# Kernel tuning notes

Measured on AMD Instinct MI355X. Metric: run time of the kernel, lower is better.

The kernel has to match this reference:

```python
import jax, jax.numpy as jnp
import numpy as np
from jax import lax

C = 768
CA = C // 4  # adapter_channels = 192
L = 197      # 1 CLS + 14*14 patches
T_FRAMES = 16
B = 16
N = B * T_FRAMES


def quick_gelu(x):
    return x * jax.nn.sigmoid(1.702 * x)


def setup_inputs() -> dict:
    key = jax.random.key(0)
    ks = jax.random.split(key, 16)
    s = 0.02
    return {
        "x": jax.random.normal(ks[0], (L, N, C), dtype=jnp.float32),
        "T": T_FRAMES,
        # main path (fc1 -> depthwise conv1d over T -> fc2)
        "fc1_w": jax.random.normal(ks[1], (C, CA), jnp.float32) * s,
        "fc1_b": jnp.zeros((CA,), jnp.float32),
        "conv_w": jax.random.normal(ks[2], (CA, 1, 3), jnp.float32) * s,  # (O, I/g, K)
        "conv_b": jnp.zeros((CA,), jnp.float32),
        "fc2_w": jax.random.normal(ks[3], (CA, C), jnp.float32) * s,
        "fc2_b": jnp.zeros((C,), jnp.float32),
        # offset adapter (fc1 -> depthwise conv3d (1,3,3) -> fc2)
        "off_fc1_w": jax.random.normal(ks[4], (C, CA), jnp.float32) * s,
        "off_fc1_b": jnp.zeros((CA,), jnp.float32),
        "off_conv_w": jax.random.normal(ks[5], (CA, 1, 1, 3, 3), jnp.float32) * s,  # (O, I/g, D, H, W)
        "off_conv_b": jnp.zeros((CA,), jnp.float32),
        "off_fc2_w": jax.random.normal(ks[6], (CA, C), jnp.float32) * s,
        "off_fc2_b": jnp.zeros((C,), jnp.float32),
        # mlp branch (c_in -> QuickGELU -> c_out)
        "mlp_in_w": jax.random.normal(ks[7], (C, CA), jnp.float32) * s,
        "mlp_in_b": jnp.zeros((CA,), jnp.float32),
        "mlp_out_w": jax.random.normal(ks[8], (CA, C), jnp.float32) * s,
        "mlp_out_b": jnp.zeros((C,), jnp.float32),
    }


def _offset_adapter(x, T, fc1_w, fc1_b, conv_w, conv_b, fc2_w, fc2_b):
    Lx, Nx, Cx = x.shape
    Bx = Nx // T
    HW = Lx - 1
    H = int(round(HW ** 0.5))
    Ca = fc1_w.shape[1]
    xp = jnp.transpose(x, (1, 0, 2))            # (N, L, C)
    xs = xp[:, 1:, :].reshape(Bx, T, HW, Cx)    # (B, T, HW, C)
    # former frame: index [0, 0, 1, ..., T-2]
    x_former = jnp.concatenate([xs[:, :1], xs[:, :-1]], axis=1)
    off = xs - x_former
    off = off @ fc1_w + fc1_b                   # (B, T, HW, Ca)
    off = off.reshape(Bx, T, H, H, Ca).transpose(0, 4, 1, 2, 3)  # (B, Ca, T, H, W)
    off = lax.conv_general_dilated(
        off, conv_w, window_strides=(1, 1, 1),
        padding=[(0, 0), (1, 1), (1, 1)],
        dimension_numbers=("NCDHW", "OIDHW", "NCDHW"),
        feature_group_count=Ca,
    ) + conv_b[None, :, None, None, None]
    off = off.transpose(0, 2, 3, 4, 1).reshape(Nx, HW, Ca)
    off = off @ fc2_w + fc2_b                   # (N, L-1, C)
    return jnp.transpose(off, (1, 0, 2))        # (L-1, N, C)


def reference(x, T, fc1_w, fc1_b, conv_w, conv_b, fc2_w, fc2_b,
              off_fc1_w, off_fc1_b, off_conv_w, off_conv_b, off_fc2_w, off_fc2_b,
              mlp_in_w, mlp_in_b, mlp_out_w, mlp_out_b):
    Lx, Nx, Cx = x.shape
    Bx = Nx // T
    Ca = fc1_w.shape[1]

    offset = _offset_adapter(x, T, off_fc1_w, off_fc1_b, off_conv_w, off_conv_b,
                             off_fc2_w, off_fc2_b)  # (L-1, N, C)

    # mlp identity branch
    x_id = quick_gelu(x @ mlp_in_w + mlp_in_b) @ mlp_out_w + mlp_out_b  # (L, N, C)

    # main branch: fc1 -> depthwise conv1d along T -> fc2
    h = x @ fc1_w + fc1_b                                   # (L, N, Ca)
    h = jnp.transpose(h, (1, 0, 2)).reshape(Bx, T, Lx, Ca)  # (B, T, L, Ca)
    h = h.transpose(0, 2, 3, 1).reshape(Bx * Lx, Ca, T)     # (B*L, Ca, T)
    h = lax.conv_general_dilated(
        h, conv_w, window_strides=(1,), padding=[(1, 1)],
        dimension_numbers=("NCH", "OIH", "NCH"),
        feature_group_count=Ca,
    ) + conv_b[None, :, None]
    h = h.transpose(0, 2, 1).reshape(Bx, Lx, T, Ca)
    h = h.transpose(0, 2, 1, 3).reshape(Nx, Lx, Ca)
    h = jnp.transpose(h, (1, 0, 2))                         # (L, N, Ca)
    h = h @ fc2_w + fc2_b                                   # (L, N, C)

    x_id = x_id.at[1:].add(offset)
    return h + x_id
```

## Files before the change

### kernel.cpp

```cpp
#include <hip/hip_runtime.h>

#define L_DIM 197
#define N_DIM 256
#define C_DIM 768
#define CA_DIM 192
#define M_DIM (L_DIM * N_DIM)

typedef short s16x8 __attribute__((ext_vector_type(8)));
typedef float f32x4 __attribute__((ext_vector_type(4)));

__device__ __forceinline__ unsigned short f2bf(float f) {
  unsigned x = __builtin_bit_cast(unsigned, f);
  x = (x + 0x7fffu + ((x >> 16) & 1u)) >> 16;
  return (unsigned short)x;
}
__device__ __forceinline__ float bflo(unsigned u) { return __builtin_bit_cast(float, u << 16); }
__device__ __forceinline__ float bfhi(unsigned u) { return __builtin_bit_cast(float, u & 0xffff0000u); }

__device__ __forceinline__ void unp8(uint4 v, float* f) {
  f[0] = bflo(v.x); f[1] = bfhi(v.x); f[2] = bflo(v.y); f[3] = bfhi(v.y);
  f[4] = bflo(v.z); f[5] = bfhi(v.z); f[6] = bflo(v.w); f[7] = bfhi(v.w);
}

__device__ __forceinline__ void mfma16(f32x4& acc, s16x8 a, s16x8 b) {
  asm("v_mfma_f32_16x16x32_bf16 %0, %1, %2, %0" : "+v"(acc) : "v"(a), "v"(b));
}

typedef const void __attribute__((address_space(1)))* gp_t;
typedef void __attribute__((address_space(3)))* lp_t;
__device__ __forceinline__ void gl16(const void* g, void* l) {
  __builtin_amdgcn_global_load_lds((gp_t)g, (lp_t)l, 16, 0, 0);
}

__device__ __forceinline__ int swz(int pid, int nwg) {
  const int q = nwg >> 3, r = nwg & 7, x = pid & 7, s = pid >> 3;
  return (x < r ? x * (q + 1) : r * (q + 1) + (x - r) * q) + s;
}

__global__ __launch_bounds__(256) void prep_k(
    const float* __restrict__ fc1_w, const float* __restrict__ mlp_in_w,
    const float* __restrict__ off_fc1_w, const float* __restrict__ fc2_w,
    const float* __restrict__ mlp_out_w, const float* __restrict__ off_fc2_w,
    unsigned short* __restrict__ wa, unsigned short* __restrict__ wc) {
  __shared__ float t[32][33];
  const int b = blockIdx.x;
  const int job = b / 144, tt = b - job * 144;
  const float* in = job == 0 ? fc1_w : job == 1 ? mlp_in_w : job == 2 ? off_fc1_w
                  : job == 3 ? fc2_w : job == 4 ? mlp_out_w : off_fc2_w;
  const int Cc = job < 3 ? 192 : 768;
  const int tc = Cc >> 5;
  const int tr0 = (tt / tc) << 5, tc0 = (tt - (tt / tc) * tc) << 5;
  const int lr = threadIdx.x >> 5, lc = threadIdx.x & 31;
#pragma unroll
  for (int p = 0; p < 4; p++)
    t[p * 8 + lr][lc] = in[(tr0 + p * 8 + lr) * Cc + tc0 + lc];
  __syncthreads();
#pragma unroll
  for (int p = 0; p < 4; p++) {
    const int orow = tc0 + p * 8 + lr;
    const int ocol = tr0 + lc;
    const unsigned short v = f2bf(t[lc][p * 8 + lr]);
    if (job < 3) wa[(job * 192 + orow) * 768 + ocol] = v;
    else         wc[orow * 576 + (job - 3) * 192 + ocol] = v;
  }
}

__global__ __launch_bounds__(256, 1) void gemm_a_k(
    const float* __restrict__ x, const unsigned short* __restrict__ wa,
    const float* __restrict__ fc1_b, const float* __restrict__ mlp_in_b,
    unsigned short* __restrict__ h1, unsigned short* __restrict__ hcat,
    unsigned short* __restrict__ yoff) {
  __shared__ unsigned short As[2][128 * 32];
  __shared__ unsigned short Bs[2][192 * 32];
  const int tid = threadIdx.x, lane = tid & 63, w = tid >> 6;
  const int lid = swz(blockIdx.x, 3 * 394);
  const int by = lid / 3, bx = lid - by * 3;
  const int m0 = by * 128, n0 = bx * 192;

  const int ar = tid >> 2, ac = (tid & 3) << 3;
  const float* ga = x + (m0 + ar) * C_DIM + ac;
  const int brow = w * 48 + (lane >> 2), bc = (lane & 3) << 3;
  const unsigned short* gb = wa + (n0 + brow) * C_DIM + bc;

  float4 av[4];
  auto ldA = [&](int kt) {
    const float* p = ga + kt * 32;
    av[0] = *(const float4*)p;                 av[1] = *(const float4*)(p + 4);
    av[2] = *(const float4*)(p + 64 * C_DIM);  av[3] = *(const float4*)(p + 64 * C_DIM + 4);
  };
  auto wrA = [&](int b) {
#pragma unroll
    for (int i = 0; i < 2; i++) {
      s16x8 v;
      const float4 u0 = av[2 * i], u1 = av[2 * i + 1];
      v[0] = (short)f2bf(u0.x); v[1] = (short)f2bf(u0.y);
      v[2] = (short)f2bf(u0.z); v[3] = (short)f2bf(u0.w);
      v[4] = (short)f2bf(u1.x); v[5] = (short)f2bf(u1.y);
      v[6] = (short)f2bf(u1.z); v[7] = (short)f2bf(u1.w);
      *(s16x8*)&As[b][(ar + i * 64) * 32 + ac] = v;
    }
  };
  auto stB = [&](int kt, int b) {
#pragma unroll
    for (int j = 0; j < 3; j++)
      gl16(gb + kt * 32 + j * 16 * C_DIM, &Bs[b][(brow + j * 16) * 32 + bc]);
  };

  f32x4 acc[4][6];
#pragma unroll
  for (int i = 0; i < 4; i++)
#pragma unroll
    for (int j = 0; j < 6; j++) acc[i][j] = (f32x4){0.f, 0.f, 0.f, 0.f};

  const int fr = lane & 15, fq = lane >> 4;
  const int wm = (w >> 1) * 64, wn = (w & 1) * 96;

  ldA(0); stB(0, 0); wrA(0); ldA(1);
  __syncthreads();
#pragma unroll 2
  for (int kt = 0; kt < 24; ++kt) {
    const int b = kt & 1;
    if (kt + 1 < 24) {
      stB(kt + 1, b ^ 1);
      wrA(b ^ 1);
      if (kt + 2 < 24) ldA(kt + 2);
    }
    s16x8 af[4], bfv[6];
#pragma unroll
    for (int mi = 0; mi < 4; mi++)
      af[mi] = *(const s16x8*)&As[b][(wm + mi * 16 + fr) * 32 + fq * 8];
#pragma unroll
    for (int ni = 0; ni < 6; ni++)
      bfv[ni] = *(const s16x8*)&Bs[b][(wn + ni * 16 + fr) * 32 + fq * 8];
#pragma unroll
    for (int mi = 0; mi < 4; mi++)
#pragma unroll
      for (int ni = 0; ni < 6; ni++) mfma16(acc[mi][ni], af[mi], bfv[ni]);
    __syncthreads();
  }

  unsigned short* dst; int stride;
  if (bx == 0)      { dst = h1;            stride = CA_DIM; }
  else if (bx == 1) { dst = hcat + CA_DIM; stride = 576; }
  else              { dst = yoff;          stride = CA_DIM; }
#pragma unroll
  for (int ni = 0; ni < 6; ni++) {
    const int ca = wn + ni * 16 + fr;
    const float bv = bx == 0 ? fc1_b[ca] : (bx == 1 ? mlp_in_b[ca] : 0.f);
#pragma unroll
    for (int mi = 0; mi < 4; mi++)
#pragma unroll
      for (int r = 0; r < 4; r++) {
        const int m = m0 + wm + mi * 16 + fq * 4 + r;
        float v = acc[mi][ni][r] + bv;
        if (bx == 1) v = v / (1.f + __expf(-1.702f * v));
        dst[m * stride + ca] = f2bf(v);
      }
  }
}

__global__ __launch_bounds__(256) void conv1d_k(
    const unsigned short* __restrict__ h1, const float* __restrict__ cw,
    const float* __restrict__ cb, unsigned short* __restrict__ hcat) {
  const int t0 = blockIdx.x * 256 + threadIdx.x;
  const int c8 = t0 % 24;
  const int ca0 = c8 * 8;
  float w0[8], w1[8], w2[8], bb[8];
#pragma unroll
  for (int e = 0; e < 8; e++) {
    w0[e] = cw[(ca0 + e) * 3 + 0];
    w1[e] = cw[(ca0 + e) * 3 + 1];
    w2[e] = cw[(ca0 + e) * 3 + 2];
    bb[e] = cb[ca0 + e];
  }
  int m = t0 / 24;
#pragma unroll
  for (int k = 0; k < 8; k++, m += 6304) {
    const int t = m & 15;
    const int base = m * CA_DIM + ca0;
    uint4 z; z.x = z.y = z.z = z.w = 0u;
    const uint4 cu = *(const uint4*)(h1 + base);
    const uint4 pu = (t > 0) ? *(const uint4*)(h1 + base - CA_DIM) : z;
    const uint4 nu = (t < 15) ? *(const uint4*)(h1 + base + CA_DIM) : z;
    float pf[8], cf[8], nf[8];
    unp8(pu, pf); unp8(cu, cf); unp8(nu, nf);
    unsigned o[4];
#pragma unroll
    for (int e = 0; e < 8; e += 2) {
      const float r0 = w0[e] * pf[e] + w1[e] * cf[e] + w2[e] * nf[e] + bb[e];
      const float r1 = w0[e+1] * pf[e+1] + w1[e+1] * cf[e+1] + w2[e+1] * nf[e+1] + bb[e+1];
      o[e / 2] = (unsigned)f2bf(r0) | ((unsigned)f2bf(r1) << 16);
    }
    uint4 ov; ov.x = o[0]; ov.y = o[1]; ov.z = o[2]; ov.w = o[3];
    *(uint4*)(hcat + (size_t)m * 576 + ca0) = ov;
  }
}

__global__ __launch_bounds__(256) void conv3d_k(
    const unsigned short* __restrict__ y, const float* __restrict__ b1,
    const float* __restrict__ w3, const float* __restrict__ b2,
    unsigned short* __restrict__ hcat) {
  __shared__ float ds[196 * 48];
  __shared__ float w3s[9 * 48];
  __shared__ float b2s[48];
  const int blk = blockIdx.x;
  const int n = blk >> 2, q = blk & 3;
  const int t = n & 15;
  const int ch0 = q * 48;
  const int tid = threadIdx.x;

  for (int j = tid; j < 432; j += 256) {
    const int c = j / 9, tap = j % 9;
    w3s[tap * 48 + c] = w3[(ch0 + c) * 9 + tap];
  }
  if (tid < 48) b2s[tid] = b2[ch0 + tid];

  for (int j = tid; j < 196 * 6; j += 256) {
    const int hw = j / 6, ck = j % 6;
    const int ca = ch0 + ck * 8;
    float dv[8];
    if (t > 0) {
      const unsigned short* p = y + ((size_t)(1 + hw) * 256 + n) * 192 + ca;
      float a0[8], a1[8];
      unp8(*(const uint4*)p, a0);
      unp8(*(const uint4*)(p - 192), a1);
#pragma unroll
      for (int e = 0; e < 8; e++) dv[e] = a0[e] - a1[e] + b1[ca + e];
    } else {
#pragma unroll
      for (int e = 0; e < 8; e++) dv[e] = b1[ca + e];
    }
#pragma unroll
    for (int e = 0; e < 8; e++) ds[hw * 48 + ck * 8 + e] = dv[e];
  }
  __syncthreads();

  for (int j = tid; j < 196 * 6; j += 256) {
    const int hw = j / 6, ck = j % 6;
    const int i = hw / 14, j0 = hw - i * 14;
    float acc[8];
#pragma unroll
    for (int e = 0; e < 8; e++) acc[e] = b2s[ck * 8 + e];
#pragma unroll
    for (int di = 0; di < 3; di++) {
      const int ii = i + di - 1;
      if (ii < 0 || ii >= 14) continue;
#pragma unroll
      for (int dj = 0; dj < 3; dj++) {
        const int jc = j0 + dj - 1;
        if (jc < 0 || jc >= 14) continue;
        const float* dp = &ds[(ii * 14 + jc) * 48 + ck * 8];
        const float* wp = &w3s[(di * 3 + dj) * 48 + ck * 8];
#pragma unroll
        for (int e = 0; e < 8; e++) acc[e] += wp[e] * dp[e];
      }
    }
    unsigned o[4];
#pragma unroll
    for (int e = 0; e < 8; e += 2)
      o[e / 2] = (unsigned)f2bf(acc[e]) | ((unsigned)f2bf(acc[e + 1]) << 16);
    uint4 ov; ov.x = o[0]; ov.y = o[1]; ov.z = o[2]; ov.w = o[3];
    *(uint4*)(hcat + ((size_t)(1 + hw) * 256 + n) * 576 + 384 + ch0 + ck * 8) = ov;
  }
}

__global__ __launch_bounds__(256) void zfill_k(unsigned short* __restrict__ hcat) {
  const int idx = blockIdx.x * 256 + threadIdx.x;
  const int m = idx / 24, ch = idx - (idx / 24) * 24;
  s16x8 z = (s16x8){0, 0, 0, 0, 0, 0, 0, 0};
  *(s16x8*)&hcat[m * 576 + 384 + ch * 8] = z;
}

__global__ __launch_bounds__(256, 1) void gemm_c_k(
    const unsigned short* __restrict__ hcat, const unsigned short* __restrict__ wc,
    const float* __restrict__ fc2_b, const float* __restrict__ mlp_out_b,
    const float* __restrict__ off_fc2_b, float* __restrict__ out) {
  __shared__ unsigned short As[2][128 * 32];
  __shared__ unsigned short Bs[2][128 * 32];
  const int tid = threadIdx.x, lane = tid & 63, w = tid >> 6;
  const int lid = swz(blockIdx.x, 6 * 394);
  const int by = lid / 6, bx = lid - by * 6;
  const int m0 = by * 128, n0 = bx * 128;

  const int srow = w * 32 + (lane >> 2), sc = (lane & 3) << 3;
  const unsigned short* gA = hcat + (m0 + srow) * 576 + sc;
  const unsigned short* gB = wc + (n0 + srow) * 576 + sc;
  auto stage = [&](int kt, int b) {
#pragma unroll
    for (int j = 0; j < 2; j++) {
      gl16(gA + kt * 32 + j * 16 * 576, &As[b][(srow + j * 16) * 32 + sc]);
      gl16(gB + kt * 32 + j * 16 * 576, &Bs[b][(srow + j * 16) * 32 + sc]);
    }
  };

  f32x4 acc[4][4];
#pragma unroll
  for (int i = 0; i < 4; i++)
#pragma unroll
    for (int j = 0; j < 4; j++) acc[i][j] = (f32x4){0.f, 0.f, 0.f, 0.f};

  const int fr = lane & 15, fq = lane >> 4;
  const int wm = (w >> 1) * 64, wn = (w & 1) * 64;

  stage(0, 0);
  __syncthreads();
#pragma unroll 2
  for (int kt = 0; kt < 18; ++kt) {
    const int b = kt & 1;
    if (kt + 1 < 18) stage(kt + 1, b ^ 1);
    s16x8 af[4], bfv[4];
#pragma unroll
    for (int mi = 0; mi < 4; mi++)
      af[mi] = *(const s16x8*)&As[b][(wm + mi * 16 + fr) * 32 + fq * 8];
#pragma unroll
    for (int ni = 0; ni < 4; ni++)
      bfv[ni] = *(const s16x8*)&Bs[b][(wn + ni * 16 + fr) * 32 + fq * 8];
#pragma unroll
    for (int mi = 0; mi < 4; mi++)
#pragma unroll
      for (int ni = 0; ni < 4; ni++) mfma16(acc[mi][ni], af[mi], bfv[ni]);
    __syncthreads();
  }

  float bv[4];
#pragma unroll
  for (int ni = 0; ni < 4; ni++) {
    const int c = n0 + wn + ni * 16 + fr;
    bv[ni] = fc2_b[c] + mlp_out_b[c] + (by >= 2 ? off_fc2_b[c] : 0.f);
  }
#pragma unroll
  for (int mi = 0; mi < 4; mi++)
#pragma unroll
    for (int r = 0; r < 4; r++) {
      const int m = m0 + wm + mi * 16 + fq * 4 + r;
      float* op = out + m * C_DIM + n0 + wn;
#pragma unroll
      for (int ni = 0; ni < 4; ni++) op[ni * 16 + fr] = acc[mi][ni][r] + bv[ni];
    }
}

extern "C" void kernel_launch(void* const* d_in, const int* in_sizes, int n_in,
                              void* d_out, int out_size, void* d_ws, size_t ws_size,
                              hipStream_t stream) {
  const float* x          = (const float*)d_in[0];
  const float* fc1_w      = (const float*)d_in[2];
  const float* fc1_b      = (const float*)d_in[3];
  const float* conv_w     = (const float*)d_in[4];
  const float* conv_b     = (const float*)d_in[5];
  const float* fc2_w      = (const float*)d_in[6];
  const float* fc2_b      = (const float*)d_in[7];
  const float* off_fc1_w  = (const float*)d_in[8];
  const float* off_fc1_b  = (const float*)d_in[9];
  const float* off_conv_w = (const float*)d_in[10];
  const float* off_conv_b = (const float*)d_in[11];
  const float* off_fc2_w  = (const float*)d_in[12];
  const float* off_fc2_b  = (const float*)d_in[13];
  const float* mlp_in_w   = (const float*)d_in[14];
  const float* mlp_in_b   = (const float*)d_in[15];
  const float* mlp_out_w  = (const float*)d_in[16];
  const float* mlp_out_b  = (const float*)d_in[17];
  float* out = (float*)d_out;

  char* ws = (char*)d_ws;
  const size_t IB = (size_t)M_DIM * CA_DIM * 2;
  unsigned short* h1   = (unsigned short*)(ws);
  unsigned short* yoff = (unsigned short*)(ws + IB);
  unsigned short* hcat = (unsigned short*)(ws + 2 * IB);
  unsigned short* wa   = (unsigned short*)(ws + 2 * IB + (size_t)M_DIM * 576 * 2);
  unsigned short* wc   = wa + (size_t)576 * 768;

  prep_k<<<864, 256, 0, stream>>>(fc1_w, mlp_in_w, off_fc1_w, fc2_w, mlp_out_w,
                                  off_fc2_w, wa, wc);
  gemm_a_k<<<1182, 256, 0, stream>>>(x, wa, fc1_b, mlp_in_b, h1, hcat, yoff);
  conv1d_k<<<591, 256, 0, stream>>>(h1, conv_w, conv_b, hcat);
  conv3d_k<<<1024, 256, 0, stream>>>(yoff, off_fc1_b, off_conv_w, off_conv_b, hcat);
  zfill_k<<<24, 256, 0, stream>>>(hcat);
  gemm_c_k<<<2364, 256, 0, stream>>>(hcat, wc, fc2_b, mlp_out_b, off_fc2_b, out);
}
```

Baseline: 212.8 us.

## Double GEMM K-tile to 64 and XOR-swizzle LDS layout

Both bf16 GEMM kernels now stage 64-wide K tiles instead of 32, halving the number of main-loop iterations and the barriers between them. Shared memory rows are 128 bytes with an XOR swizzle of the 16-byte column chunk by row, applied both to the direct global-to-LDS loads and to the fragment reads, to avoid bank conflicts. This doubles LDS use per block and raises register pressure for the A prefetch in gemm_a (eight float4 loads per thread). Some index math is also widened to size_t.

```diff
diff --git a/kernel.cpp b/kernel.cpp
--- a/kernel.cpp
+++ b/kernel.cpp
@@ -35,6 +35,10 @@
 __device__ __forceinline__ int swz(int pid, int nwg) {
   const int q = nwg >> 3, r = nwg & 7, x = pid & 7, s = pid >> 3;
   return (x < r ? x * (q + 1) : r * (q + 1) + (x - r) * q) + s;
+}
+
+__device__ __forceinline__ int lidx(int row, int colb) {
+  return (row * 128 + (colb ^ ((row & 7) << 4))) >> 1;
 }
 
 __global__ __launch_bounds__(256) void prep_k(
@@ -70,40 +74,44 @@
     const float* __restrict__ fc1_b, const float* __restrict__ mlp_in_b,
     unsigned short* __restrict__ h1, unsigned short* __restrict__ hcat,
     unsigned short* __restrict__ yoff) {
-  __shared__ unsigned short As[2][128 * 32];
-  __shared__ unsigned short Bs[2][192 * 32];
+  __shared__ unsigned short As[2][128 * 64];
+  __shared__ unsigned short Bs[2][192 * 64];
   const int tid = threadIdx.x, lane = tid & 63, w = tid >> 6;
   const int lid = swz(blockIdx.x, 3 * 394);
   const int by = lid / 3, bx = lid - by * 3;
   const int m0 = by * 128, n0 = bx * 192;
 
-  const int ar = tid >> 2, ac = (tid & 3) << 3;
-  const float* ga = x + (m0 + ar) * C_DIM + ac;
-  const int brow = w * 48 + (lane >> 2), bc = (lane & 3) << 3;
-  const unsigned short* gb = wa + (n0 + brow) * C_DIM + bc;
-
-  float4 av[4];
+  const int arow = tid >> 1, ahalf = tid & 1;
+  const float* ga = x + (size_t)(m0 + arow) * C_DIM + ahalf * 32;
+  const int lrow8 = lane >> 3;
+  const int csw = (((lane & 7) ^ lrow8) << 4);
+  const char* gbB = (const char*)wa +
+      (size_t)2 * (n0 + w * 48 + lrow8) * C_DIM + csw;
+
+  float4 av[8];
   auto ldA = [&](int kt) {
-    const float* p = ga + kt * 32;
-    av[0] = *(const float4*)p;                 av[1] = *(const float4*)(p + 4);
-    av[2] = *(const float4*)(p + 64 * C_DIM);  av[3] = *(const float4*)(p + 64 * C_DIM + 4);
+    const float* p = ga + kt * 64;
+#pragma unroll
+    for (int j = 0; j < 8; j++) av[j] = *(const float4*)(p + j * 4);
   };
   auto wrA = [&](int b) {
 #pragma unroll
-    for (int i = 0; i < 2; i++) {
+    for (int jj = 0; jj < 4; jj++) {
       s16x8 v;
-      const float4 u0 = av[2 * i], u1 = av[2 * i + 1];
+      const float4 u0 = av[2 * jj], u1 = av[2 * jj + 1];
       v[0] = (short)f2bf(u0.x); v[1] = (short)f2bf(u0.y);
       v[2] = (short)f2bf(u0.z); v[3] = (short)f2bf(u0.w);
       v[4] = (short)f2bf(u1.x); v[5] = (short)f2bf(u1.y);
       v[6] = (short)f2bf(u1.z); v[7] = (short)f2bf(u1.w);
-      *(s16x8*)&As[b][(ar + i * 64) * 32 + ac] = v;
+      *(s16x8*)&As[b][lidx(arow, ahalf * 64 + jj * 16)] = v;
     }
   };
   auto stB = [&](int kt, int b) {
-#pragma unroll
-    for (int j = 0; j < 3; j++)
-      gl16(gb + kt * 32 + j * 16 * C_DIM, &Bs[b][(brow + j * 16) * 32 + bc]);
+    char* lb = (char*)&Bs[b][0] + w * 6144 + lane * 16;
+    const char* gb = gbB + kt * 128;
+#pragma unroll
+    for (int j = 0; j < 6; j++)
+      gl16(gb + j * (8 * C_DIM * 2), lb + j * 1024);
   };
 
   f32x4 acc[4][6];
@@ -115,27 +123,29 @@
   const int fr = lane & 15, fq = lane >> 4;
   const int wm = (w >> 1) * 64, wn = (w & 1) * 96;
 
-  ldA(0); stB(0, 0); wrA(0); ldA(1);
+  ldA(0); wrA(0); stB(0, 0); ldA(1);
   __syncthreads();
-#pragma unroll 2
-  for (int kt = 0; kt < 24; ++kt) {
+  for (int kt = 0; kt < 12; ++kt) {
     const int b = kt & 1;
-    if (kt + 1 < 24) {
+    if (kt + 1 < 12) {
       stB(kt + 1, b ^ 1);
       wrA(b ^ 1);
-      if (kt + 2 < 24) ldA(kt + 2);
-    }
-    s16x8 af[4], bfv[6];
-#pragma unroll
-    for (int mi = 0; mi < 4; mi++)
-      af[mi] = *(const s16x8*)&As[b][(wm + mi * 16 + fr) * 32 + fq * 8];
-#pragma unroll
-    for (int ni = 0; ni < 6; ni++)
-      bfv[ni] = *(const s16x8*)&Bs[b][(wn + ni * 16 + fr) * 32 + fq * 8];
-#pragma unroll
-    for (int mi = 0; mi < 4; mi++)
-#pragma unroll
-      for (int ni = 0; ni < 6; ni++) mfma16(acc[mi][ni], af[mi], bfv[ni]);
+      if (kt + 2 < 12) ldA(kt + 2);
+    }
+#pragma unroll
+    for (int kk = 0; kk < 2; ++kk) {
+      s16x8 af[4], bfv[6];
+#pragma unroll
+      for (int mi = 0; mi < 4; mi++)
+        af[mi] = *(const s16x8*)&As[b][lidx(wm + mi * 16 + fr, kk * 64 + fq * 16)];
+#pragma unroll
+      for (int ni = 0; ni < 6; ni++)
+        bfv[ni] = *(const s16x8*)&Bs[b][lidx(wn + ni * 16 + fr, kk * 64 + fq * 16)];
+#pragma unroll
+      for (int mi = 0; mi < 4; mi++)
+#pragma unroll
+        for (int ni = 0; ni < 6; ni++) mfma16(acc[mi][ni], af[mi], bfv[ni]);
+    }
     __syncthreads();
   }
 
@@ -154,7 +164,7 @@
         const int m = m0 + wm + mi * 16 + fq * 4 + r;
         float v = acc[mi][ni][r] + bv;
         if (bx == 1) v = v / (1.f + __expf(-1.702f * v));
-        dst[m * stride + ca] = f2bf(v);
+        dst[(size_t)m * stride + ca] = f2bf(v);
       }
   }
 }
@@ -275,21 +285,27 @@
     const unsigned short* __restrict__ hcat, const unsigned short* __restrict__ wc,
     const float* __restrict__ fc2_b, const float* __restrict__ mlp_out_b,
     const float* __restrict__ off_fc2_b, float* __restrict__ out) {
-  __shared__ unsigned short As[2][128 * 32];
-  __shared__ unsigned short Bs[2][128 * 32];
+  __shared__ unsigned short As[2][128 * 64];
+  __shared__ unsigned short Bs[2][128 * 64];
   const int tid = threadIdx.x, lane = tid & 63, w = tid >> 6;
   const int lid = swz(blockIdx.x, 6 * 394);
   const int by = lid / 6, bx = lid - by * 6;
   const int m0 = by * 128, n0 = bx * 128;
 
-  const int srow = w * 32 + (lane >> 2), sc = (lane & 3) << 3;
-  const unsigned short* gA = hcat + (m0 + srow) * 576 + sc;
-  const unsigned short* gB = wc + (n0 + srow) * 576 + sc;
+  const int lrow8 = lane >> 3;
+  const int csw = (((lane & 7) ^ lrow8) << 4);
+  const char* gAb = (const char*)hcat + (size_t)2 * (m0 + w * 32 + lrow8) * 576 + csw;
+  const char* gBb = (const char*)wc   + (size_t)2 * (n0 + w * 32 + lrow8) * 576 + csw;
+
   auto stage = [&](int kt, int b) {
-#pragma unroll
-    for (int j = 0; j < 2; j++) {
-      gl16(gA + kt * 32 + j * 16 * 576, &As[b][(srow + j * 16) * 32 + sc]);
-      gl16(gB + kt * 32 + j * 16 * 576, &Bs[b][(srow + j * 16) * 32 + sc]);
+    char* la = (char*)&As[b][0] + w * 4096 + lane * 16;
+    char* lb = (char*)&Bs[b][0] + w * 4096 + lane * 16;
+    const char* ga = gAb + kt * 128;
+    const char* gb = gBb + kt * 128;
+#pragma unroll
+    for (int j = 0; j < 4; j++) {
+      gl16(ga + j * (8 * 576 * 2), la + j * 1024);
+      gl16(gb + j * (8 * 576 * 2), lb + j * 1024);
     }
   };
 
@@ -304,21 +320,23 @@
 
   stage(0, 0);
   __syncthreads();
-#pragma unroll 2
-  for (int kt = 0; kt < 18; ++kt) {
+  for (int kt = 0; kt < 9; ++kt) {
     const int b = kt & 1;
-    if (kt + 1 < 18) stage(kt + 1, b ^ 1);
-    s16x8 af[4], bfv[4];
-#pragma unroll
-    for (int mi = 0; mi < 4; mi++)
-      af[mi] = *(const s16x8*)&As[b][(wm + mi * 16 + fr) * 32 + fq * 8];
-#pragma unroll
-    for (int ni = 0; ni < 4; ni++)
-      bfv[ni] = *(const s16x8*)&Bs[b][(wn + ni * 16 + fr) * 32 + fq * 8];
-#pragma unroll
-    for (int mi = 0; mi < 4; mi++)
-#pragma unroll
-      for (int ni = 0; ni < 4; ni++) mfma16(acc[mi][ni], af[mi], bfv[ni]);
+    if (kt + 1 < 9) stage(kt + 1, b ^ 1);
+#pragma unroll
+    for (int kk = 0; kk < 2; ++kk) {
+      s16x8 af[4], bfv[4];
+#pragma unroll
+      for (int mi = 0; mi < 4; mi++)
+        af[mi] = *(const s16x8*)&As[b][lidx(wm + mi * 16 + fr, kk * 64 + fq * 16)];
+#pragma unroll
+      for (int ni = 0; ni < 4; ni++)
+        bfv[ni] = *(const s16x8*)&Bs[b][lidx(wn + ni * 16 + fr, kk * 64 + fq * 16)];
+#pragma unroll
+      for (int mi = 0; mi < 4; mi++)
+#pragma unroll
+        for (int ni = 0; ni < 4; ni++) mfma16(acc[mi][ni], af[mi], bfv[ni]);
+    }
     __syncthreads();
   }
 
@@ -333,7 +351,7 @@
 #pragma unroll
     for (int r = 0; r < 4; r++) {
       const int m = m0 + wm + mi * 16 + fq * 4 + r;
-      float* op = out + m * C_DIM + n0 + wn;
+      float* op = out + (size_t)m * C_DIM + n0 + wn;
 #pragma unroll
       for (int ni = 0; ni < 4; ni++) op[ni * 16 + fr] = acc[mi][ni][r] + bv[ni];
     }
```

Result: slower. 246.1 us (+15.7%).

## Use 512-thread blocks with 8 waves in both GEMM kernels

Applied to the files above, without the earlier changes.

Both GEMM kernels move from 4 to 8 waves per 128-row tile. Each wave now owns half as many output columns, and global-to-LDS staging is redistributed so each thread issues fewer loads. Launch bounds go from (256,1) to (512,4), so more waves fit per CU to hide memory latency. In exchange, per-wave operand reuse drops, the A fragments are read from LDS by twice as many waves, and the explicit unroll-by-2 is removed.

```diff
diff --git a/kernel.cpp b/kernel.cpp
--- a/kernel.cpp
+++ b/kernel.cpp
@@ -65,7 +65,7 @@
   }
 }
 
-__global__ __launch_bounds__(256, 1) void gemm_a_k(
+__global__ __launch_bounds__(512, 4) void gemm_a_k(
     const float* __restrict__ x, const unsigned short* __restrict__ wa,
     const float* __restrict__ fc1_b, const float* __restrict__ mlp_in_b,
     unsigned short* __restrict__ h1, unsigned short* __restrict__ hcat,
@@ -78,46 +78,40 @@
   const int m0 = by * 128, n0 = bx * 192;
 
   const int ar = tid >> 2, ac = (tid & 3) << 3;
-  const float* ga = x + (m0 + ar) * C_DIM + ac;
-  const int brow = w * 48 + (lane >> 2), bc = (lane & 3) << 3;
-  const unsigned short* gb = wa + (n0 + brow) * C_DIM + bc;
-
-  float4 av[4];
+  const float* ga = x + (size_t)(m0 + ar) * C_DIM + ac;
+  const unsigned short* gb0 = wa + (size_t)(n0 + ar) * C_DIM + ac;
+  const unsigned short* gb1 = wa + (size_t)(n0 + 128 + ar) * C_DIM + ac;
+
+  float4 av[2];
   auto ldA = [&](int kt) {
     const float* p = ga + kt * 32;
-    av[0] = *(const float4*)p;                 av[1] = *(const float4*)(p + 4);
-    av[2] = *(const float4*)(p + 64 * C_DIM);  av[3] = *(const float4*)(p + 64 * C_DIM + 4);
+    av[0] = *(const float4*)p;
+    av[1] = *(const float4*)(p + 4);
   };
   auto wrA = [&](int b) {
-#pragma unroll
-    for (int i = 0; i < 2; i++) {
-      s16x8 v;
-      const float4 u0 = av[2 * i], u1 = av[2 * i + 1];
-      v[0] = (short)f2bf(u0.x); v[1] = (short)f2bf(u0.y);
-      v[2] = (short)f2bf(u0.z); v[3] = (short)f2bf(u0.w);
-      v[4] = (short)f2bf(u1.x); v[5] = (short)f2bf(u1.y);
-      v[6] = (short)f2bf(u1.z); v[7] = (short)f2bf(u1.w);
-      *(s16x8*)&As[b][(ar + i * 64) * 32 + ac] = v;
-    }
+    s16x8 v;
+    v[0] = (short)f2bf(av[0].x); v[1] = (short)f2bf(av[0].y);
+    v[2] = (short)f2bf(av[0].z); v[3] = (short)f2bf(av[0].w);
+    v[4] = (short)f2bf(av[1].x); v[5] = (short)f2bf(av[1].y);
+    v[6] = (short)f2bf(av[1].z); v[7] = (short)f2bf(av[1].w);
+    *(s16x8*)&As[b][ar * 32 + ac] = v;
   };
   auto stB = [&](int kt, int b) {
-#pragma unroll
-    for (int j = 0; j < 3; j++)
-      gl16(gb + kt * 32 + j * 16 * C_DIM, &Bs[b][(brow + j * 16) * 32 + bc]);
+    gl16(gb0 + kt * 32, &Bs[b][ar * 32 + ac]);
+    if (tid < 256) gl16(gb1 + kt * 32, &Bs[b][(128 + ar) * 32 + ac]);
   };
 
-  f32x4 acc[4][6];
+  f32x4 acc[4][3];
 #pragma unroll
   for (int i = 0; i < 4; i++)
 #pragma unroll
-    for (int j = 0; j < 6; j++) acc[i][j] = (f32x4){0.f, 0.f, 0.f, 0.f};
+    for (int j = 0; j < 3; j++) acc[i][j] = (f32x4){0.f, 0.f, 0.f, 0.f};
 
   const int fr = lane & 15, fq = lane >> 4;
-  const int wm = (w >> 1) * 64, wn = (w & 1) * 96;
-
-  ldA(0); stB(0, 0); wrA(0); ldA(1);
+  const int wm = (w >> 2) * 64, wn = (w & 3) * 48;
+
+  ldA(0); wrA(0); stB(0, 0); ldA(1);
   __syncthreads();
-#pragma unroll 2
   for (int kt = 0; kt < 24; ++kt) {
     const int b = kt & 1;
     if (kt + 1 < 24) {
@@ -125,17 +119,17 @@
       wrA(b ^ 1);
       if (kt + 2 < 24) ldA(kt + 2);
     }
-    s16x8 af[4], bfv[6];
+    s16x8 af[4], bfv[3];
 #pragma unroll
     for (int mi = 0; mi < 4; mi++)
       af[mi] = *(const s16x8*)&As[b][(wm + mi * 16 + fr) * 32 + fq * 8];
 #pragma unroll
-    for (int ni = 0; ni < 6; ni++)
+    for (int ni = 0; ni < 3; ni++)
       bfv[ni] = *(const s16x8*)&Bs[b][(wn + ni * 16 + fr) * 32 + fq * 8];
 #pragma unroll
     for (int mi = 0; mi < 4; mi++)
 #pragma unroll
-      for (int ni = 0; ni < 6; ni++) mfma16(acc[mi][ni], af[mi], bfv[ni]);
+      for (int ni = 0; ni < 3; ni++) mfma16(acc[mi][ni], af[mi], bfv[ni]);
     __syncthreads();
   }
 
@@ -144,7 +138,7 @@
   else if (bx == 1) { dst = hcat + CA_DIM; stride = 576; }
   else              { dst = yoff;          stride = CA_DIM; }
 #pragma unroll
-  for (int ni = 0; ni < 6; ni++) {
+  for (int ni = 0; ni < 3; ni++) {
     const int ca = wn + ni * 16 + fr;
     const float bv = bx == 0 ? fc1_b[ca] : (bx == 1 ? mlp_in_b[ca] : 0.f);
 #pragma unroll
@@ -154,7 +148,7 @@
         const int m = m0 + wm + mi * 16 + fq * 4 + r;
         float v = acc[mi][ni][r] + bv;
         if (bx == 1) v = v / (1.f + __expf(-1.702f * v));
-        dst[m * stride + ca] = f2bf(v);
+        dst[(size_t)m * stride + ca] = f2bf(v);
       }
   }
 }
@@ -271,7 +265,7 @@
   *(s16x8*)&hcat[m * 576 + 384 + ch * 8] = z;
 }
 
-__global__ __launch_bounds__(256, 1) void gemm_c_k(
+__global__ __launch_bounds__(512, 4) void gemm_c_k(
     const unsigned short* __restrict__ hcat, const unsigned short* __restrict__ wc,
     const float* __restrict__ fc2_b, const float* __restrict__ mlp_out_b,
     const float* __restrict__ off_fc2_b, float* __restrict__ out) {
@@ -282,49 +276,45 @@
   const int by = lid / 6, bx = lid - by * 6;
   const int m0 = by * 128, n0 = bx * 128;
 
-  const int srow = w * 32 + (lane >> 2), sc = (lane & 3) << 3;
-  const unsigned short* gA = hcat + (m0 + srow) * 576 + sc;
-  const unsigned short* gB = wc + (n0 + srow) * 576 + sc;
+  const int sr = tid >> 2, sc = (tid & 3) << 3;
+  const unsigned short* gA = hcat + (size_t)(m0 + sr) * 576 + sc;
+  const unsigned short* gB = wc + (size_t)(n0 + sr) * 576 + sc;
   auto stage = [&](int kt, int b) {
-#pragma unroll
-    for (int j = 0; j < 2; j++) {
-      gl16(gA + kt * 32 + j * 16 * 576, &As[b][(srow + j * 16) * 32 + sc]);
-      gl16(gB + kt * 32 + j * 16 * 576, &Bs[b][(srow + j * 16) * 32 + sc]);
-    }
+    gl16(gA + kt * 32, &As[b][sr * 32 + sc]);
+    gl16(gB + kt * 32, &Bs[b][sr * 32 + sc]);
   };
 
-  f32x4 acc[4][4];
+  f32x4 acc[4][2];
 #pragma unroll
   for (int i = 0; i < 4; i++)
 #pragma unroll
-    for (int j = 0; j < 4; j++) acc[i][j] = (f32x4){0.f, 0.f, 0.f, 0.f};
+    for (int j = 0; j < 2; j++) acc[i][j] = (f32x4){0.f, 0.f, 0.f, 0.f};
 
   const int fr = lane & 15, fq = lane >> 4;
-  const int wm = (w >> 1) * 64, wn = (w & 1) * 64;
+  const int wm = (w >> 2) * 64, wn = (w & 3) * 32;
 
   stage(0, 0);
   __syncthreads();
-#pragma unroll 2
   for (int kt = 0; kt < 18; ++kt) {
     const int b = kt & 1;
     if (kt + 1 < 18) stage(kt + 1, b ^ 1);
-    s16x8 af[4], bfv[4];
+    s16x8 af[4], bfv[2];
 #pragma unroll
     for (int mi = 0; mi < 4; mi++)
       af[mi] = *(const s16x8*)&As[b][(wm + mi * 16 + fr) * 32 + fq * 8];
 #pragma unroll
-    for (int ni = 0; ni < 4; ni++)
+    for (int ni = 0; ni < 2; ni++)
       bfv[ni] = *(const s16x8*)&Bs[b][(wn + ni * 16 + fr) * 32 + fq * 8];
 #pragma unroll
     for (int mi = 0; mi < 4; mi++)
 #pragma unroll
-      for (int ni = 0; ni < 4; ni++) mfma16(acc[mi][ni], af[mi], bfv[ni]);
+      for (int ni = 0; ni < 2; ni++) mfma16(acc[mi][ni], af[mi], bfv[ni]);
     __syncthreads();
   }
 
-  float bv[4];
-#pragma unroll
-  for (int ni = 0; ni < 4; ni++) {
+  float bv[2];
+#pragma unroll
+  for (int ni = 0; ni < 2; ni++) {
     const int c = n0 + wn + ni * 16 + fr;
     bv[ni] = fc2_b[c] + mlp_out_b[c] + (by >= 2 ? off_fc2_b[c] : 0.f);
   }
@@ -333,9 +323,9 @@
 #pragma unroll
     for (int r = 0; r < 4; r++) {
       const int m = m0 + wm + mi * 16 + fq * 4 + r;
-      float* op = out + m * C_DIM + n0 + wn;
-#pragma unroll
-      for (int ni = 0; ni < 4; ni++) op[ni * 16 + fr] = acc[mi][ni][r] + bv[ni];
+      float* op = out + (size_t)m * C_DIM + n0 + wn;
+#pragma unroll
+      for (int ni = 0; ni < 2; ni++) op[ni * 16 + fr] = acc[mi][ni][r] + bv[ni];
     }
 }
 
@@ -371,9 +361,9 @@
 
   prep_k<<<864, 256, 0, stream>>>(fc1_w, mlp_in_w, off_fc1_w, fc2_w, mlp_out_w,
                                   off_fc2_w, wa, wc);
-  gemm_a_k<<<1182, 256, 0, stream>>>(x, wa, fc1_b, mlp_in_b, h1, hcat, yoff);
+  gemm_a_k<<<1182, 512, 0, stream>>>(x, wa, fc1_b, mlp_in_b, h1, hcat, yoff);
   conv1d_k<<<591, 256, 0, stream>>>(h1, conv_w, conv_b, hcat);
   conv3d_k<<<1024, 256, 0, stream>>>(yoff, off_fc1_b, off_conv_w, off_conv_b, hcat);
   zfill_k<<<24, 256, 0, stream>>>(hcat);
-  gemm_c_k<<<2364, 256, 0, stream>>>(hcat, wc, fc2_b, mlp_out_b, off_fc2_b, out);
-}
+  gemm_c_k<<<2364, 512, 0, stream>>>(hcat, wc, fc2_b, mlp_out_b, off_fc2_b, out);
+}
```

Result: slower. 231.6 us (+8.8%).

## Fuse temporal conv and frame difference into GEMM epilogue, pre-convert x to bf16

Applied to the files above, without the earlier changes.

Adds a separate kernel that converts x to bf16 once, so gemm_a can stage A tiles with direct async global-to-LDS loads instead of doing register loads and in-loop conversion. The depthwise temporal conv1d and the offset frame-difference are moved into the gemm_a epilogue using cross-lane shuffles, because each 16-row fragment holds 16 consecutive frames. This removes the conv1d kernel and the h1/yoff intermediate buffers. The cost is an extra full pass over x (read fp32, write bf16) and more epilogue work.

```diff
diff --git a/kernel.cpp b/kernel.cpp
--- a/kernel.cpp
+++ b/kernel.cpp
@@ -65,11 +65,27 @@
   }
 }
 
+__global__ __launch_bounds__(256) void xcvt_k(const float* __restrict__ x,
+                                              unsigned short* __restrict__ xb) {
+  const int total8 = M_DIM * C_DIM / 8;
+  const int step = gridDim.x * 256;
+  for (int i = blockIdx.x * 256 + threadIdx.x; i < total8; i += step) {
+    const float4 a = *(const float4*)(x + (size_t)i * 8);
+    const float4 b = *(const float4*)(x + (size_t)i * 8 + 4);
+    s16x8 v;
+    v[0] = (short)f2bf(a.x); v[1] = (short)f2bf(a.y);
+    v[2] = (short)f2bf(a.z); v[3] = (short)f2bf(a.w);
+    v[4] = (short)f2bf(b.x); v[5] = (short)f2bf(b.y);
+    v[6] = (short)f2bf(b.z); v[7] = (short)f2bf(b.w);
+    *(s16x8*)(xb + (size_t)i * 8) = v;
+  }
+}
+
 __global__ __launch_bounds__(256, 1) void gemm_a_k(
-    const float* __restrict__ x, const unsigned short* __restrict__ wa,
+    const unsigned short* __restrict__ xb, const unsigned short* __restrict__ wa,
     const float* __restrict__ fc1_b, const float* __restrict__ mlp_in_b,
-    unsigned short* __restrict__ h1, unsigned short* __restrict__ hcat,
-    unsigned short* __restrict__ yoff) {
+    const float* __restrict__ cw, const float* __restrict__ cb,
+    const float* __restrict__ off_b1, unsigned short* __restrict__ hcat) {
   __shared__ unsigned short As[2][128 * 32];
   __shared__ unsigned short Bs[2][192 * 32];
   const int tid = threadIdx.x, lane = tid & 63, w = tid >> 6;
@@ -77,33 +93,18 @@
   const int by = lid / 3, bx = lid - by * 3;
   const int m0 = by * 128, n0 = bx * 192;
 
-  const int ar = tid >> 2, ac = (tid & 3) << 3;
-  const float* ga = x + (m0 + ar) * C_DIM + ac;
-  const int brow = w * 48 + (lane >> 2), bc = (lane & 3) << 3;
-  const unsigned short* gb = wa + (n0 + brow) * C_DIM + bc;
-
-  float4 av[4];
-  auto ldA = [&](int kt) {
-    const float* p = ga + kt * 32;
-    av[0] = *(const float4*)p;                 av[1] = *(const float4*)(p + 4);
-    av[2] = *(const float4*)(p + 64 * C_DIM);  av[3] = *(const float4*)(p + 64 * C_DIM + 4);
-  };
-  auto wrA = [&](int b) {
-#pragma unroll
-    for (int i = 0; i < 2; i++) {
-      s16x8 v;
-      const float4 u0 = av[2 * i], u1 = av[2 * i + 1];
-      v[0] = (short)f2bf(u0.x); v[1] = (short)f2bf(u0.y);
-      v[2] = (short)f2bf(u0.z); v[3] = (short)f2bf(u0.w);
-      v[4] = (short)f2bf(u1.x); v[5] = (short)f2bf(u1.y);
-      v[6] = (short)f2bf(u1.z); v[7] = (short)f2bf(u1.w);
-      *(s16x8*)&As[b][(ar + i * 64) * 32 + ac] = v;
-    }
-  };
-  auto stB = [&](int kt, int b) {
-#pragma unroll
-    for (int j = 0; j < 3; j++)
-      gl16(gb + kt * 32 + j * 16 * C_DIM, &Bs[b][(brow + j * 16) * 32 + bc]);
+  const int sr = tid >> 2, sc = (tid & 3) * 8;
+  const unsigned short* gA0 = xb + (size_t)(m0 + sr) * C_DIM + sc;
+  const unsigned short* gA1 = xb + (size_t)(m0 + 64 + sr) * C_DIM + sc;
+  const unsigned short* gB = wa + (size_t)(n0 + sr) * C_DIM + sc;
+
+  auto stage = [&](int kt, int b) {
+    gl16(gA0 + kt * 32, &As[b][sr * 32 + sc]);
+    gl16(gA1 + kt * 32, &As[b][(64 + sr) * 32 + sc]);
+    const unsigned short* pb = gB + kt * 32;
+    gl16(pb,               &Bs[b][sr * 32 + sc]);
+    gl16(pb + 64 * C_DIM,  &Bs[b][(64 + sr) * 32 + sc]);
+    gl16(pb + 128 * C_DIM, &Bs[b][(128 + sr) * 32 + sc]);
   };
 
   f32x4 acc[4][6];
@@ -115,16 +116,11 @@
   const int fr = lane & 15, fq = lane >> 4;
   const int wm = (w >> 1) * 64, wn = (w & 1) * 96;
 
-  ldA(0); stB(0, 0); wrA(0); ldA(1);
+  stage(0, 0);
   __syncthreads();
-#pragma unroll 2
   for (int kt = 0; kt < 24; ++kt) {
     const int b = kt & 1;
-    if (kt + 1 < 24) {
-      stB(kt + 1, b ^ 1);
-      wrA(b ^ 1);
-      if (kt + 2 < 24) ldA(kt + 2);
-    }
+    if (kt + 1 < 24) stage(kt + 1, b ^ 1);
     s16x8 af[4], bfv[6];
 #pragma unroll
     for (int mi = 0; mi < 4; mi++)
@@ -139,65 +135,65 @@
     __syncthreads();
   }
 
-  unsigned short* dst; int stride;
-  if (bx == 0)      { dst = h1;            stride = CA_DIM; }
-  else if (bx == 1) { dst = hcat + CA_DIM; stride = 576; }
-  else              { dst = yoff;          stride = CA_DIM; }
-#pragma unroll
-  for (int ni = 0; ni < 6; ni++) {
-    const int ca = wn + ni * 16 + fr;
-    const float bv = bx == 0 ? fc1_b[ca] : (bx == 1 ? mlp_in_b[ca] : 0.f);
-#pragma unroll
-    for (int mi = 0; mi < 4; mi++)
-#pragma unroll
-      for (int r = 0; r < 4; r++) {
-        const int m = m0 + wm + mi * 16 + fq * 4 + r;
-        float v = acc[mi][ni][r] + bv;
-        if (bx == 1) v = v / (1.f + __expf(-1.702f * v));
-        dst[m * stride + ca] = f2bf(v);
+  if (bx == 0) {
+#pragma unroll
+    for (int ni = 0; ni < 6; ni++) {
+      const int ca = wn + ni * 16 + fr;
+      const float bv = fc1_b[ca];
+      const float w0 = cw[ca * 3], w1 = cw[ca * 3 + 1], w2 = cw[ca * 3 + 2];
+      const float cbv = cb[ca];
+#pragma unroll
+      for (int mi = 0; mi < 4; mi++) {
+        const float v0 = acc[mi][ni][0] + bv, v1 = acc[mi][ni][1] + bv;
+        const float v2 = acc[mi][ni][2] + bv, v3 = acc[mi][ni][3] + bv;
+        const float pv3 = __shfl_up(v3, 16);
+        const float nv0 = __shfl_down(v0, 16);
+        const float p0 = fq > 0 ? pv3 : 0.f;
+        const float n3 = fq < 3 ? nv0 : 0.f;
+        const int mb = m0 + wm + mi * 16 + fq * 4;
+        hcat[(size_t)(mb + 0) * 576 + ca] = f2bf(w0 * p0 + w1 * v0 + w2 * v1 + cbv);
+        hcat[(size_t)(mb + 1) * 576 + ca] = f2bf(w0 * v0 + w1 * v1 + w2 * v2 + cbv);
+        hcat[(size_t)(mb + 2) * 576 + ca] = f2bf(w0 * v1 + w1 * v2 + w2 * v3 + cbv);
+        hcat[(size_t)(mb + 3) * 576 + ca] = f2bf(w0 * v2 + w1 * v3 + w2 * n3 + cbv);
       }
-  }
-}
-
-__global__ __launch_bounds__(256) void conv1d_k(
-    const unsigned short* __restrict__ h1, const float* __restrict__ cw,
-    const float* __restrict__ cb, unsigned short* __restrict__ hcat) {
-  const int t0 = blockIdx.x * 256 + threadIdx.x;
-  const int c8 = t0 % 24;
-  const int ca0 = c8 * 8;
-  float w0[8], w1[8], w2[8], bb[8];
-#pragma unroll
-  for (int e = 0; e < 8; e++) {
-    w0[e] = cw[(ca0 + e) * 3 + 0];
-    w1[e] = cw[(ca0 + e) * 3 + 1];
-    w2[e] = cw[(ca0 + e) * 3 + 2];
-    bb[e] = cb[ca0 + e];
-  }
-  int m = t0 / 24;
-#pragma unroll
-  for (int k = 0; k < 8; k++, m += 6304) {
-    const int t = m & 15;
-    const int base = m * CA_DIM + ca0;
-    uint4 z; z.x = z.y = z.z = z.w = 0u;
-    const uint4 cu = *(const uint4*)(h1 + base);
-    const uint4 pu = (t > 0) ? *(const uint4*)(h1 + base - CA_DIM) : z;
-    const uint4 nu = (t < 15) ? *(const uint4*)(h1 + base + CA_DIM) : z;
-    float pf[8], cf[8], nf[8];
-    unp8(pu, pf); unp8(cu, cf); unp8(nu, nf);
-    unsigned o[4];
-#pragma unroll
-    for (int e = 0; e < 8; e += 2) {
-      const float r0 = w0[e] * pf[e] + w1[e] * cf[e] + w2[e] * nf[e] + bb[e];
-      const float r1 = w0[e+1] * pf[e+1] + w1[e+1] * cf[e+1] + w2[e+1] * nf[e+1] + bb[e+1];
-      o[e / 2] = (unsigned)f2bf(r0) | ((unsigned)f2bf(r1) << 16);
-    }
-    uint4 ov; ov.x = o[0]; ov.y = o[1]; ov.z = o[2]; ov.w = o[3];
-    *(uint4*)(hcat + (size_t)m * 576 + ca0) = ov;
+    }
+  } else if (bx == 1) {
+#pragma unroll
+    for (int ni = 0; ni < 6; ni++) {
+      const int ca = wn + ni * 16 + fr;
+      const float bv = mlp_in_b[ca];
+#pragma unroll
+      for (int mi = 0; mi < 4; mi++)
+#pragma unroll
+        for (int r = 0; r < 4; r++) {
+          const int m = m0 + wm + mi * 16 + fq * 4 + r;
+          float v = acc[mi][ni][r] + bv;
+          v = v / (1.f + __expf(-1.702f * v));
+          hcat[(size_t)m * 576 + 192 + ca] = f2bf(v);
+        }
+    }
+  } else {
+#pragma unroll
+    for (int ni = 0; ni < 6; ni++) {
+      const int ca = wn + ni * 16 + fr;
+      const float bv = off_b1[ca];
+#pragma unroll
+      for (int mi = 0; mi < 4; mi++) {
+        const float v0 = acc[mi][ni][0], v1 = acc[mi][ni][1];
+        const float v2 = acc[mi][ni][2], v3 = acc[mi][ni][3];
+        const float pv3 = __shfl_up(v3, 16);
+        const int mb = m0 + wm + mi * 16 + fq * 4;
+        const float o0 = (fq == 0) ? bv : (v0 - pv3 + bv);
+        hcat[(size_t)(mb + 0) * 576 + 384 + ca] = f2bf(o0);
+        hcat[(size_t)(mb + 1) * 576 + 384 + ca] = f2bf(v1 - v0 + bv);
+        hcat[(size_t)(mb + 2) * 576 + 384 + ca] = f2bf(v2 - v1 + bv);
+        hcat[(size_t)(mb + 3) * 576 + 384 + ca] = f2bf(v3 - v2 + bv);
+      }
+    }
   }
 }
 
 __global__ __launch_bounds__(256) void conv3d_k(
-    const unsigned short* __restrict__ y, const float* __restrict__ b1,
     const float* __restrict__ w3, const float* __restrict__ b2,
     unsigned short* __restrict__ hcat) {
   __shared__ float ds[196 * 48];
@@ -205,7 +201,6 @@
   __shared__ float b2s[48];
   const int blk = blockIdx.x;
   const int n = blk >> 2, q = blk & 3;
-  const int t = n & 15;
   const int ch0 = q * 48;
   const int tid = threadIdx.x;
 
@@ -217,19 +212,8 @@
 
   for (int j = tid; j < 196 * 6; j += 256) {
     const int hw = j / 6, ck = j % 6;
-    const int ca = ch0 + ck * 8;
     float dv[8];
-    if (t > 0) {
-      const unsigned short* p = y + ((size_t)(1 + hw) * 256 + n) * 192 + ca;
-      float a0[8], a1[8];
-      unp8(*(const uint4*)p, a0);
-      unp8(*(const uint4*)(p - 192), a1);
-#pragma unroll
-      for (int e = 0; e < 8; e++) dv[e] = a0[e] - a1[e] + b1[ca + e];
-    } else {
-#pragma unroll
-      for (int e = 0; e < 8; e++) dv[e] = b1[ca + e];
-    }
+    unp8(*(const uint4*)(hcat + ((size_t)(1 + hw) * 256 + n) * 576 + 384 + ch0 + ck * 8), dv);
 #pragma unroll
     for (int e = 0; e < 8; e++) ds[hw * 48 + ck * 8 + e] = dv[e];
   }
@@ -268,7 +252,7 @@
   const int idx = blockIdx.x * 256 + threadIdx.x;
   const int m = idx / 24, ch = idx - (idx / 24) * 24;
   s16x8 z = (s16x8){0, 0, 0, 0, 0, 0, 0, 0};
-  *(s16x8*)&hcat[m * 576 + 384 + ch * 8] = z;
+  *(s16x8*)&hcat[(size_t)m * 576 + 384 + ch * 8] = z;
 }
 
 __global__ __launch_bounds__(256, 1) void gemm_c_k(
@@ -283,8 +267,8 @@
   const int m0 = by * 128, n0 = bx * 128;
 
   const int srow = w * 32 + (lane >> 2), sc = (lane & 3) << 3;
-  const unsigned short* gA = hcat + (m0 + srow) * 576 + sc;
-  const unsigned short* gB = wc + (n0 + srow) * 576 + sc;
+  const unsigned short* gA = hcat + (size_t)(m0 + srow) * 576 + sc;
+  const unsigned short* gB = wc + (size_t)(n0 + srow) * 576 + sc;
   auto stage = [&](int kt, int b) {
 #pragma unroll
     for (int j = 0; j < 2; j++) {
@@ -304,7 +288,6 @@
 
   stage(0, 0);
   __syncthreads();
-#pragma unroll 2
   for (int kt = 0; kt < 18; ++kt) {
     const int b = kt & 1;
     if (kt + 1 < 18) stage(kt + 1, b ^ 1);
@@ -333,7 +316,7 @@
 #pragma unroll
     for (int r = 0; r < 4; r++) {
       const int m = m0 + wm + mi * 16 + fq * 4 + r;
-      float* op = out + m * C_DIM + n0 + wn;
+      float* op = out + (size_t)m * C_DIM + n0 + wn;
 #pragma unroll
       for (int ni = 0; ni < 4; ni++) op[ni * 16 + fr] = acc[mi][ni][r] + bv[ni];
     }
@@ -362,18 +345,18 @@
   float* out = (float*)d_out;
 
   char* ws = (char*)d_ws;
-  const size_t IB = (size_t)M_DIM * CA_DIM * 2;
-  unsigned short* h1   = (unsigned short*)(ws);
-  unsigned short* yoff = (unsigned short*)(ws + IB);
-  unsigned short* hcat = (unsigned short*)(ws + 2 * IB);
-  unsigned short* wa   = (unsigned short*)(ws + 2 * IB + (size_t)M_DIM * 576 * 2);
+  unsigned short* xb   = (unsigned short*)(ws);
+  unsigned short* hcat = (unsigned short*)(ws + (size_t)M_DIM * C_DIM * 2);
+  unsigned short* wa   = (unsigned short*)(ws + (size_t)M_DIM * C_DIM * 2
+                                              + (size_t)M_DIM * 576 * 2);
   unsigned short* wc   = wa + (size_t)576 * 768;
 
   prep_k<<<864, 256, 0, stream>>>(fc1_w, mlp_in_w, off_fc1_w, fc2_w, mlp_out_w,
                                   off_fc2_w, wa, wc);
-  gemm_a_k<<<1182, 256, 0, stream>>>(x, wa, fc1_b, mlp_in_b, h1, hcat, yoff);
-  conv1d_k<<<591, 256, 0, stream>>>(h1, conv_w, conv_b, hcat);
-  conv3d_k<<<1024, 256, 0, stream>>>(yoff, off_fc1_b, off_conv_w, off_conv_b, hcat);
+  xcvt_k<<<2048, 256, 0, stream>>>(x, xb);
+  gemm_a_k<<<1182, 256, 0, stream>>>(xb, wa, fc1_b, mlp_in_b, conv_w, conv_b,
+                                     off_fc1_b, hcat);
   zfill_k<<<24, 256, 0, stream>>>(hcat);
+  conv3d_k<<<1024, 256, 0, stream>>>(off_conv_w, off_conv_b, hcat);
   gemm_c_k<<<2364, 256, 0, stream>>>(hcat, wc, fc2_b, mlp_out_b, off_fc2_b, out);
 }
```

New measurement: 219.6 us. 3.2% more time.
